# Optimization experiments

Measured on AMD Instinct MI355X. Metric: run time of the kernel, lower is better.

## Reference

```python
import jax, jax.numpy as jnp
import numpy as np

HINGES = 8_000_000
SHIMS = 2
L = 1.0


def setup_inputs() -> dict:
    key = jax.random.key(0)
    k1, k2, k3 = jax.random.split(key, 3)
    # straight chain [[0,0],[1,0],...] + small perturbation (as in _initiate_pos)
    x = jnp.arange(HINGES + 2, dtype=jnp.float32)
    base = jnp.stack([x, jnp.zeros_like(x)], axis=1)
    pos_arr = base + 0.01 * jax.random.normal(k1, (HINGES + 2, 2), dtype=jnp.float32)
    thetas_ss = 0.3 * jax.random.uniform(k2, (HINGES,), dtype=jnp.float32)
    rest_lengths = jnp.full((HINGES + 1,), L, dtype=jnp.float32)
    # buckle in {-1, +1}
    buckle = (2 * jax.random.randint(k3, (HINGES, SHIMS), 0, 2) - 1).astype(jnp.int32)
    return {
        "pos_arr": pos_arr,
        "thetas_ss": thetas_ss,
        "rest_lengths": rest_lengths,
        "k_stiff": jnp.asarray(10.0, dtype=jnp.float32),
        "k_soft": jnp.asarray(0.1, dtype=jnp.float32),
        "k_stretch": jnp.asarray(100.0, dtype=jnp.float32),
        "buckle": buckle,
    }


def _energy(pos, thetas_ss, rest_lengths, k_stiff, k_soft, k_stretch, buckle):
    # hinge angles: signed angle between consecutive edge vectors (vmap'd _get_theta)
    v1 = pos[1:-1] - pos[:-2]   # (H, 2)
    v2 = pos[2:] - pos[1:-1]    # (H, 2)
    cross = v1[:, 0] * v2[:, 1] - v1[:, 1] * v2[:, 0]
    dot = jnp.sum(v1 * v2, axis=-1)
    thetas = jnp.arctan2(cross, dot)             # (H,)
    # edge lengths (vmap'd _get_edge_length), edges = hinges + 1
    ev = pos[1:] - pos[:-1]
    edge_len = jnp.sqrt(jnp.sum(ev * ev, axis=-1))  # (H+1,)

    T = thetas[:, None]          # (H, 1)
    TH = thetas_ss[:, None]      # (H, 1)
    B = buckle                   # (H, shims)
    stiff_mask = ((B == 1) & (T > -TH)) | ((B == -1) & (T < TH))
    k_rot = jnp.where(stiff_mask, k_stiff, k_soft)
    rot_e = 0.5 * jnp.sum(k_rot * (T - TH) ** 2)
    str_e = 0.5 * jnp.sum(k_stretch * (edge_len - rest_lengths) ** 2)
    return rot_e + str_e, rot_e, str_e


def reference(pos_arr, thetas_ss, rest_lengths, k_stiff, k_soft, k_stretch, buckle):
    n_coords = pos_arr.size
    # nodes 0 and 1 (DOFs 0..3) are constrained per calculate_state
    free = jnp.ones((n_coords,), dtype=bool).at[:4].set(False)

    def total_E(x_flat):
        p = x_flat.reshape(pos_arr.shape)
        return _energy(p, thetas_ss, rest_lengths, k_stiff, k_soft, k_stretch, buckle)[0]

    g = jax.grad(total_E)(pos_arr.reshape(-1))
    force = jnp.where(free, -g, 0.0)             # -dE/dx on free DOFs

    tot, rot, st = _energy(pos_arr, thetas_ss, rest_lengths, k_stiff, k_soft, k_stretch, buckle)
    energies = jnp.stack([tot, rot, st])
    return jnp.concatenate([energies, force])
```

## Files before the change

### kernel.cpp

```cpp
#include <hip/hip_runtime.h>
#include <math.h>

#define TILE 256

__device__ __forceinline__ float fast_rcp(float x)  { return __builtin_amdgcn_rcpf(x); }
__device__ __forceinline__ float fast_rsq(float x)  { return __builtin_amdgcn_rsqf(x); }

__device__ __forceinline__ float atan_poly(float t) {
    const float c3 = -0.3333333333f, c5 = 0.2f, c7 = -0.1428571429f, c9 = 0.1111111111f;
    float t2 = t * t;
    return t * fmaf(t2, fmaf(t2, fmaf(t2, fmaf(t2, c9, c7), c5), c3), 1.0f);
}

__global__ __launch_bounds__(TILE) void hinge_chain_kernel(
    const float2* __restrict__ pos,
    const float*  __restrict__ thetas_ss,
    const float*  __restrict__ rest_len,
    const float*  __restrict__ k_stiff_p,
    const float*  __restrict__ k_soft_p,
    const float*  __restrict__ k_stretch_p,
    const int2*   __restrict__ buckle,
    float*        __restrict__ out,
    float2*       __restrict__ partials,
    int N)
{
    const int H = N - 2;
    const int E = N - 1;
    const int tid  = threadIdx.x;
    const int base = blockIdx.x * TILE;

    __shared__ float2 lpos[TILE + 4];
    __shared__ float2 lgv1[TILE + 2];
    __shared__ float2 lgv2[TILE + 2];
    __shared__ float2 ls  [TILE + 1];

    const float k_stiff   = *k_stiff_p;
    const float k_soft    = *k_soft_p;
    const float k_stretch = *k_stretch_p;

    for (int i = tid; i < TILE + 4; i += TILE) {
        int p = base - 2 + i;
        float2 v = make_float2(0.f, 0.f);
        if (p >= 0 && p < N) v = pos[p];
        lpos[i] = v;
    }
    __syncthreads();

    float rot_e = 0.f;
    float str_e = 0.f;

    for (int i = tid; i < TILE + 2; i += TILE) {
        int h = base - 2 + i;
        float2 g1 = make_float2(0.f, 0.f);
        float2 g2 = make_float2(0.f, 0.f);
        if (h >= 0 && h < H) {
            float2 p0 = lpos[i], p1 = lpos[i + 1], p2 = lpos[i + 2];
            float v1x = p1.x - p0.x, v1y = p1.y - p0.y;
            float v2x = p2.x - p1.x, v2y = p2.y - p1.y;
            float cr = v1x * v2y - v1y * v2x;
            float dt = v1x * v2x + v1y * v2y;
            float th;
            if (dt > 0.f) {
                th = atan_poly(cr * fast_rcp(dt));
            } else {
                th = atan2f(cr, dt);
            }
            float tss = thetas_ss[h];
            int2  b  = buckle[h];
            float dth = th - tss;
            bool m0 = (b.x == 1 && th > -tss) || (b.x == -1 && th < tss);
            bool m1 = (b.y == 1 && th > -tss) || (b.y == -1 && th < tss);
            float K = (m0 ? k_stiff : k_soft) + (m1 ? k_stiff : k_soft);
            rot_e += 0.5f * K * dth * dth;
            float gg  = K * dth;
            float inv = gg * fast_rcp(cr * cr + dt * dt);
            g1.x = inv * ( dt * v2y - cr * v2x);
            g1.y = inv * (-dt * v2x - cr * v2y);
            g2.x = inv * (-dt * v1y - cr * v1x);
            g2.y = inv * ( dt * v1x - cr * v1y);
        }
        lgv1[i] = g1;
        lgv2[i] = g2;
    }

    for (int i = tid; i < TILE + 1; i += TILE) {
        int e = base - 1 + i;
        float2 s = make_float2(0.f, 0.f);
        if (e >= 0 && e < E) {
            float2 p0 = lpos[i + 1], p1 = lpos[i + 2];
            float ex = p1.x - p0.x, ey = p1.y - p0.y;
            float d2     = ex * ex + ey * ey;
            float invlen = fast_rsq(d2);
            float len    = d2 * invlen;
            float rl  = rest_len[e];
            float d   = len - rl;
            str_e += 0.5f * k_stretch * d * d;
            float c = k_stretch * d * invlen;
            s.x = c * ex;
            s.y = c * ey;
        }
        ls[i] = s;
    }
    __syncthreads();

    int p = base + tid;
    if (p < N) {
        float gx = 0.f, gy = 0.f;
        gx -= lgv1[tid + 2].x;  gy -= lgv1[tid + 2].y;
        gx += lgv1[tid + 1].x - lgv2[tid + 1].x;
        gy += lgv1[tid + 1].y - lgv2[tid + 1].y;
        gx += lgv2[tid].x;      gy += lgv2[tid].y;
        gx += ls[tid].x;        gy += ls[tid].y;
        gx -= ls[tid + 1].x;    gy -= ls[tid + 1].y;

        float fx = -gx, fy = -gy;
        if (p < 2) { fx = 0.f; fy = 0.f; }
        out[3 + 2 * p]     = fx;
        out[3 + 2 * p + 1] = fy;
    }

    for (int off = 32; off > 0; off >>= 1) {
        rot_e += __shfl_down(rot_e, off);
        str_e += __shfl_down(str_e, off);
    }
    __shared__ float wr[TILE / 64], wsum[TILE / 64];
    int wave = tid >> 6, lane = tid & 63;
    if (lane == 0) { wr[wave] = rot_e; wsum[wave] = str_e; }
    __syncthreads();
    if (tid == 0) {
        float r = 0.f, s = 0.f;
        for (int w = 0; w < TILE / 64; ++w) { r += wr[w]; s += wsum[w]; }
        partials[blockIdx.x] = make_float2(r, s);
    }
}

__global__ __launch_bounds__(256) void reduce_partials_kernel(
    const float2* __restrict__ partials, int nblocks,
    float* __restrict__ out)
{
    const int tid = threadIdx.x;
    float r0 = 0.f, s0 = 0.f, r1 = 0.f, s1 = 0.f;
    int i = tid;
    for (; i + 256 < nblocks; i += 512) {
        float2 a = partials[i];
        float2 b = partials[i + 256];
        r0 += a.x; s0 += a.y;
        r1 += b.x; s1 += b.y;
    }
    if (i < nblocks) { float2 a = partials[i]; r0 += a.x; s0 += a.y; }
    float r = r0 + r1, s = s0 + s1;
    for (int off = 32; off > 0; off >>= 1) {
        r += __shfl_down(r, off);
        s += __shfl_down(s, off);
    }
    __shared__ float wr[4], wsv[4];
    int wave = tid >> 6, lane = tid & 63;
    if (lane == 0) { wr[wave] = r; wsv[wave] = s; }
    __syncthreads();
    if (tid == 0) {
        float R = 0.f, S = 0.f;
        for (int w = 0; w < 4; ++w) { R += wr[w]; S += wsv[w]; }
        out[0] = R + S;
        out[1] = R;
        out[2] = S;
    }
}

extern "C" void kernel_launch(void* const* d_in, const int* in_sizes, int n_in,
                              void* d_out, int out_size, void* d_ws, size_t ws_size,
                              hipStream_t stream) {
    const float2* pos       = (const float2*)d_in[0];
    const float*  thetas_ss = (const float*)d_in[1];
    const float*  rest_len  = (const float*)d_in[2];
    const float*  k_stiff   = (const float*)d_in[3];
    const float*  k_soft    = (const float*)d_in[4];
    const float*  k_stretch = (const float*)d_in[5];
    const int2*   buckle    = (const int2*)d_in[6];
    float*        out       = (float*)d_out;
    float2*       partials  = (float2*)d_ws;

    const int N = in_sizes[0] / 2;
    const int grid = (N + TILE - 1) / TILE;

    hinge_chain_kernel<<<grid, TILE, 0, stream>>>(
        pos, thetas_ss, rest_len, k_stiff, k_soft, k_stretch, buckle, out, partials, N);

    reduce_partials_kernel<<<1, 256, 0, stream>>>(partials, grid, out);
}
```

Before: 249.9 us.

## Process four nodes per thread in registers with vectorized loads, dropping LDS staging

```diff
diff --git a/kernel.cpp b/kernel.cpp
--- a/kernel.cpp
+++ b/kernel.cpp
@@ -2,9 +2,10 @@
 #include <math.h>
 
 #define TILE 256
-
-__device__ __forceinline__ float fast_rcp(float x)  { return __builtin_amdgcn_rcpf(x); }
-__device__ __forceinline__ float fast_rsq(float x)  { return __builtin_amdgcn_rsqf(x); }
+#define PPT  4
+
+__device__ __forceinline__ float fast_rcp(float x) { return __builtin_amdgcn_rcpf(x); }
+__device__ __forceinline__ float fast_rsq(float x) { return __builtin_amdgcn_rsqf(x); }
 
 __device__ __forceinline__ float atan_poly(float t) {
     const float c3 = -0.3333333333f, c5 = 0.2f, c7 = -0.1428571429f, c9 = 0.1111111111f;
@@ -26,97 +27,124 @@
 {
     const int H = N - 2;
     const int E = N - 1;
-    const int tid  = threadIdx.x;
-    const int base = blockIdx.x * TILE;
-
-    __shared__ float2 lpos[TILE + 4];
-    __shared__ float2 lgv1[TILE + 2];
-    __shared__ float2 lgv2[TILE + 2];
-    __shared__ float2 ls  [TILE + 1];
+    const int gid = blockIdx.x * TILE + threadIdx.x;
+    const int p0  = gid * PPT;
 
     const float k_stiff   = *k_stiff_p;
     const float k_soft    = *k_soft_p;
     const float k_stretch = *k_stretch_p;
 
-    for (int i = tid; i < TILE + 4; i += TILE) {
-        int p = base - 2 + i;
-        float2 v = make_float2(0.f, 0.f);
-        if (p >= 0 && p < N) v = pos[p];
-        lpos[i] = v;
-    }
-    __syncthreads();
-
-    float rot_e = 0.f;
-    float str_e = 0.f;
-
-    for (int i = tid; i < TILE + 2; i += TILE) {
-        int h = base - 2 + i;
-        float2 g1 = make_float2(0.f, 0.f);
-        float2 g2 = make_float2(0.f, 0.f);
-        if (h >= 0 && h < H) {
-            float2 p0 = lpos[i], p1 = lpos[i + 1], p2 = lpos[i + 2];
-            float v1x = p1.x - p0.x, v1y = p1.y - p0.y;
-            float v2x = p2.x - p1.x, v2y = p2.y - p1.y;
+    float2 P[8];
+    float  tss[6];
+    int2   bb[6];
+    float  rl[5];
+
+    const bool interior = (p0 >= 2) && (p0 + 5 < N);
+    if (interior) {
+        const float4* p4 = reinterpret_cast<const float4*>(pos + (p0 - 2));
+        float4 a = p4[0], b = p4[1], c = p4[2], d = p4[3];
+        P[0] = make_float2(a.x, a.y); P[1] = make_float2(a.z, a.w);
+        P[2] = make_float2(b.x, b.y); P[3] = make_float2(b.z, b.w);
+        P[4] = make_float2(c.x, c.y); P[5] = make_float2(c.z, c.w);
+        P[6] = make_float2(d.x, d.y); P[7] = make_float2(d.z, d.w);
+        float2 t01 = *reinterpret_cast<const float2*>(thetas_ss + (p0 - 2));
+        float4 t25 = *reinterpret_cast<const float4*>(thetas_ss + p0);
+        tss[0] = t01.x; tss[1] = t01.y;
+        tss[2] = t25.x; tss[3] = t25.y; tss[4] = t25.z; tss[5] = t25.w;
+        rl[0] = rest_len[p0 - 1];
+        float4 r14 = *reinterpret_cast<const float4*>(rest_len + p0);
+        rl[1] = r14.x; rl[2] = r14.y; rl[3] = r14.z; rl[4] = r14.w;
+        const int4* b4 = reinterpret_cast<const int4*>(buckle + (p0 - 2));
+        int4 u = b4[0], v = b4[1], w = b4[2];
+        bb[0] = make_int2(u.x, u.y); bb[1] = make_int2(u.z, u.w);
+        bb[2] = make_int2(v.x, v.y); bb[3] = make_int2(v.z, v.w);
+        bb[4] = make_int2(w.x, w.y); bb[5] = make_int2(w.z, w.w);
+    } else {
+        #pragma unroll
+        for (int j = 0; j < 8; ++j) {
+            int p = p0 - 2 + j;
+            P[j] = (p >= 0 && p < N) ? pos[p] : make_float2(0.f, 0.f);
+        }
+        #pragma unroll
+        for (int j = 0; j < 6; ++j) {
+            int h = p0 - 2 + j;
+            bool v = (h >= 0 && h < H);
+            tss[j] = v ? thetas_ss[h] : 0.f;
+            bb[j]  = v ? buckle[h]    : make_int2(0, 0);
+        }
+        #pragma unroll
+        for (int k = 0; k < 5; ++k) {
+            int e = p0 - 1 + k;
+            rl[k] = (e >= 0 && e < E) ? rest_len[e] : 1.f;
+        }
+    }
+
+    float rot_e = 0.f, str_e = 0.f;
+
+    float2 g1[6], g2[6];
+    #pragma unroll
+    for (int j = 0; j < 6; ++j) {
+        int h = p0 - 2 + j;
+        bool valid = (h >= 0 && h < H);
+        if (valid) {
+            float2 a = P[j], b = P[j + 1], c = P[j + 2];
+            float v1x = b.x - a.x, v1y = b.y - a.y;
+            float v2x = c.x - b.x, v2y = c.y - b.y;
             float cr = v1x * v2y - v1y * v2x;
             float dt = v1x * v2x + v1y * v2y;
             float th;
-            if (dt > 0.f) {
-                th = atan_poly(cr * fast_rcp(dt));
-            } else {
-                th = atan2f(cr, dt);
-            }
-            float tss = thetas_ss[h];
-            int2  b  = buckle[h];
-            float dth = th - tss;
-            bool m0 = (b.x == 1 && th > -tss) || (b.x == -1 && th < tss);
-            bool m1 = (b.y == 1 && th > -tss) || (b.y == -1 && th < tss);
+            if (dt > 0.f) th = atan_poly(cr * fast_rcp(dt));
+            else          th = atan2f(cr, dt);
+            float ts  = tss[j];
+            int2  bk  = bb[j];
+            float dth = th - ts;
+            bool m0 = (bk.x == 1 && th > -ts) || (bk.x == -1 && th < ts);
+            bool m1 = (bk.y == 1 && th > -ts) || (bk.y == -1 && th < ts);
             float K = (m0 ? k_stiff : k_soft) + (m1 ? k_stiff : k_soft);
-            rot_e += 0.5f * K * dth * dth;
+            if (j >= 2) rot_e += 0.5f * K * dth * dth;
             float gg  = K * dth;
             float inv = gg * fast_rcp(cr * cr + dt * dt);
-            g1.x = inv * ( dt * v2y - cr * v2x);
-            g1.y = inv * (-dt * v2x - cr * v2y);
-            g2.x = inv * (-dt * v1y - cr * v1x);
-            g2.y = inv * ( dt * v1x - cr * v1y);
-        }
-        lgv1[i] = g1;
-        lgv2[i] = g2;
-    }
-
-    for (int i = tid; i < TILE + 1; i += TILE) {
-        int e = base - 1 + i;
-        float2 s = make_float2(0.f, 0.f);
-        if (e >= 0 && e < E) {
-            float2 p0 = lpos[i + 1], p1 = lpos[i + 2];
-            float ex = p1.x - p0.x, ey = p1.y - p0.y;
-            float d2     = ex * ex + ey * ey;
-            float invlen = fast_rsq(d2);
-            float len    = d2 * invlen;
-            float rl  = rest_len[e];
-            float d   = len - rl;
-            str_e += 0.5f * k_stretch * d * d;
-            float c = k_stretch * d * invlen;
-            s.x = c * ex;
-            s.y = c * ey;
-        }
-        ls[i] = s;
-    }
-    __syncthreads();
-
-    int p = base + tid;
-    if (p < N) {
-        float gx = 0.f, gy = 0.f;
-        gx -= lgv1[tid + 2].x;  gy -= lgv1[tid + 2].y;
-        gx += lgv1[tid + 1].x - lgv2[tid + 1].x;
-        gy += lgv1[tid + 1].y - lgv2[tid + 1].y;
-        gx += lgv2[tid].x;      gy += lgv2[tid].y;
-        gx += ls[tid].x;        gy += ls[tid].y;
-        gx -= ls[tid + 1].x;    gy -= ls[tid + 1].y;
-
-        float fx = -gx, fy = -gy;
-        if (p < 2) { fx = 0.f; fy = 0.f; }
-        out[3 + 2 * p]     = fx;
-        out[3 + 2 * p + 1] = fy;
+            g1[j].x = inv * ( dt * v2y - cr * v2x);
+            g1[j].y = inv * (-dt * v2x - cr * v2y);
+            g2[j].x = inv * (-dt * v1y - cr * v1x);
+            g2[j].y = inv * ( dt * v1x - cr * v1y);
+        } else {
+            g1[j] = make_float2(0.f, 0.f);
+            g2[j] = make_float2(0.f, 0.f);
+        }
+    }
+
+    float2 s[5];
+    #pragma unroll
+    for (int k = 0; k < 5; ++k) {
+        int e = p0 - 1 + k;
+        bool valid = (e >= 0 && e < E);
+        if (valid) {
+            float2 a = P[k + 1], b = P[k + 2];
+            float ex = b.x - a.x, ey = b.y - a.y;
+            float d2 = ex * ex + ey * ey;
+            float invl = fast_rsq(d2);
+            float len  = d2 * invl;
+            float d    = len - rl[k];
+            if (k >= 1) str_e += 0.5f * k_stretch * d * d;
+            float cc = k_stretch * d * invl;
+            s[k] = make_float2(cc * ex, cc * ey);
+        } else {
+            s[k] = make_float2(0.f, 0.f);
+        }
+    }
+
+    #pragma unroll
+    for (int m = 0; m < 4; ++m) {
+        int p = p0 + m;
+        if (p < N) {
+            float gx = -g1[m + 2].x + g1[m + 1].x - g2[m + 1].x + g2[m].x + s[m].x - s[m + 1].x;
+            float gy = -g1[m + 2].y + g1[m + 1].y - g2[m + 1].y + g2[m].y + s[m].y - s[m + 1].y;
+            float fx = -gx, fy = -gy;
+            if (p < 2) { fx = 0.f; fy = 0.f; }
+            out[3 + 2 * p]     = fx;
+            out[4 + 2 * p]     = fy;
+        }
     }
 
     for (int off = 32; off > 0; off >>= 1) {
@@ -124,13 +152,13 @@
         str_e += __shfl_down(str_e, off);
     }
     __shared__ float wr[TILE / 64], wsum[TILE / 64];
-    int wave = tid >> 6, lane = tid & 63;
+    int wave = threadIdx.x >> 6, lane = threadIdx.x & 63;
     if (lane == 0) { wr[wave] = rot_e; wsum[wave] = str_e; }
     __syncthreads();
-    if (tid == 0) {
-        float r = 0.f, s = 0.f;
-        for (int w = 0; w < TILE / 64; ++w) { r += wr[w]; s += wsum[w]; }
-        partials[blockIdx.x] = make_float2(r, s);
+    if (threadIdx.x == 0) {
+        float r = 0.f, ss = 0.f;
+        for (int w = 0; w < TILE / 64; ++w) { r += wr[w]; ss += wsum[w]; }
+        partials[blockIdx.x] = make_float2(r, ss);
     }
 }
 
@@ -180,7 +208,8 @@
     float2*       partials  = (float2*)d_ws;
 
     const int N = in_sizes[0] / 2;
-    const int grid = (N + TILE - 1) / TILE;
+    const int nthreads = (N + PPT - 1) / PPT;
+    const int grid = (nthreads + TILE - 1) / TILE;
 
     hinge_chain_kernel<<<grid, TILE, 0, stream>>>(
         pos, thetas_ss, rest_len, k_stiff, k_soft, k_stretch, buckle, out, partials, N);
```

New measurement: 222.1 us. 1.13x faster.
